# Kernel tuning notes

Hardware: AMD Instinct MI355X
Metric: run time of the kernel (lower is better)

## Reference

```python
import jax, jax.numpy as jnp
import numpy as np

NUM_ATTRS = 8    # A: number of attribute names in attr_map
NUM_VALS = 16    # V: number of distinct values per attribute


def setup_inputs() -> dict:
    key = jax.random.key(0)
    k1, k2 = jax.random.split(key)
    B, D = 2_000_000, 8
    predictions = jax.random.normal(k1, (B, D), dtype=jnp.float32)
    attr_vals = jax.random.randint(k2, (B, NUM_ATTRS), 0, NUM_VALS, dtype=jnp.int32)
    return {"predictions": predictions, "attr_vals": attr_vals}


def reference(predictions, attr_vals):
    B, A = attr_vals.shape
    V = NUM_VALS
    # per-node mean of sigmoid probs; stacking rows then .mean() == mean of per-node means
    per_node = jnp.mean(jax.nn.sigmoid(predictions), axis=1)  # [B]
    # flatten (attr, value) groups into A*V segments
    seg_ids = (attr_vals + jnp.arange(A, dtype=attr_vals.dtype)[None, :] * V).reshape(-1)  # [B*A]
    vals = jnp.broadcast_to(per_node[:, None], (B, A)).reshape(-1)  # [B*A]
    sums = jax.ops.segment_sum(vals, seg_ids, num_segments=A * V)
    counts = jax.ops.segment_sum(jnp.ones_like(vals), seg_ids, num_segments=A * V)
    means = (sums / jnp.maximum(counts, 1.0)).reshape(A, V)      # [A, V]
    present = (counts > 0).reshape(A, V)                          # [A, V]
    # pairwise squared diffs of group means within each attribute (i < j)
    diff = means[:, :, None] - means[:, None, :]                  # [A, V, V]
    triu = jnp.triu(jnp.ones((V, V), dtype=bool), k=1)
    pair_mask = present[:, :, None] & present[:, None, :] & triu[None, :, :]
    total_loss = jnp.sum(jnp.where(pair_mask, diff * diff, 0.0))
    num_comparisons = jnp.sum(pair_mask)
    return jnp.where(num_comparisons > 0, total_loss / num_comparisons, 0.0)
```

## Files before the change

### kernel.cpp

```cpp
#include <hip/hip_runtime.h>

#define NA 8
#define NV 16
#define NS (NA * NV)
#define NW 4
#define FIX_SHIFT 43
#define FIX_MASK ((1ULL << FIX_SHIFT) - 1)
#define FIX_SCALE 2147483648.0f


__device__ __forceinline__ float sig(float x) {
    return __builtin_amdgcn_rcpf(1.0f + __expf(-x));
}

__device__ __forceinline__ void process_chunk(
    float4 p, int4 a, int lane, unsigned long long* __restrict__ hw)
{
    float hs = sig(p.x) + sig(p.y) + sig(p.z) + sig(p.w);
    float s  = hs + __shfl_xor(hs, 1, 64);
    float per_node = s * 0.125f;
    unsigned int fixed = (unsigned int)(per_node * FIX_SCALE);
    unsigned long long add = (1ULL << FIX_SHIFT) | (unsigned long long)fixed;
    const int abase = (lane & 1) << 2;
    atomicAdd(&hw[((abase + 0) << 4) + a.x], add);
    atomicAdd(&hw[((abase + 1) << 4) + a.y], add);
    atomicAdd(&hw[((abase + 2) << 4) + a.z], add);
    atomicAdd(&hw[((abase + 3) << 4) + a.w], add);
}

__global__ __launch_bounds__(256) void k1_accum(
    const float* __restrict__ preds,
    const int*   __restrict__ attrs,
    unsigned long long* __restrict__ partials,
    int B, int nb)
{
    __shared__ unsigned long long h[NW][NS];
    for (int i = threadIdx.x; i < NW * NS; i += 256)
        ((unsigned long long*)h)[i] = 0ULL;
    __syncthreads();

    const int lane = threadIdx.x & 63;
    const int wave = threadIdx.x >> 6;
    unsigned long long* __restrict__ hw = h[wave];

    const float4* __restrict__ p4 = (const float4*)preds;
    const int4*   __restrict__ a4 = (const int4*)attrs;

    const int gw      = blockIdx.x * NW + wave;
    const int nwv     = nb * NW;
    const int nchunks = B >> 5;

    int c = gw;
    if (c < nchunks) {
        float4 p = p4[(size_t)c * 64 + lane];
        int4   a = a4[(size_t)c * 64 + lane];
        for (;;) {
            const int  cn   = c + nwv;
            const bool more = (cn < nchunks);
            float4 pn; int4 an;
            if (more) {
                pn = p4[(size_t)cn * 64 + lane];
                an = a4[(size_t)cn * 64 + lane];
            }
            process_chunk(p, a, lane, hw);
            if (!more) break;
            p = pn; a = an; c = cn;
        }
    }

    const int rem = B & 31;
    if (rem && blockIdx.x == 0 && wave == 0 && lane < rem * 2) {
        const size_t base = (size_t)(B >> 5) * 64;
        float4 p = p4[base + lane];
        int4   a = a4[base + lane];
        process_chunk(p, a, lane, hw);
    }
    __syncthreads();

    if (threadIdx.x < NS) {
        unsigned long long m = h[0][threadIdx.x] + h[1][threadIdx.x]
                             + h[2][threadIdx.x] + h[3][threadIdx.x];
        partials[(size_t)threadIdx.x * nb + blockIdx.x] = m;
    }
}

__global__ __launch_bounds__(256) void k2_reduce(
    const unsigned long long* __restrict__ partials,
    double* __restrict__ means,
    int*    __restrict__ pres,
    int nb)
{
    const int s = blockIdx.x;
    unsigned long long sum = 0ULL;
    unsigned int cnt = 0u;
    for (int b = threadIdx.x; b < nb; b += 256) {
        unsigned long long p = partials[(size_t)s * nb + b];
        cnt += (unsigned int)(p >> FIX_SHIFT);
        sum += (p & FIX_MASK);
    }
    for (int off = 32; off > 0; off >>= 1) {
        sum += __shfl_down(sum, off, 64);
        cnt += __shfl_down(cnt, off, 64);
    }
    __shared__ unsigned long long ws_[4];
    __shared__ unsigned int wc_[4];
    const int wave = threadIdx.x >> 6;
    if ((threadIdx.x & 63) == 0) { ws_[wave] = sum; wc_[wave] = cnt; }
    __syncthreads();
    if (threadIdx.x == 0) {
        unsigned long long S = ws_[0] + ws_[1] + ws_[2] + ws_[3];
        unsigned int C = wc_[0] + wc_[1] + wc_[2] + wc_[3];
        means[s] = C ? ((double)S * (1.0 / (double)FIX_SCALE)) / (double)C : 0.0;
        pres[s]  = C ? 1 : 0;
    }
}

__global__ __launch_bounds__(128) void k3_finalize(
    const double* __restrict__ means,
    const int*    __restrict__ pres,
    float* __restrict__ out)
{
    __shared__ double s_mean[NS];
    __shared__ int    s_pres[NS];
    const int t = threadIdx.x;
    s_mean[t] = means[t];
    s_pres[t] = pres[t];
    __syncthreads();

    const int a = t >> 4;
    const int i = t & (NV - 1);
    double loss = 0.0;
    int    ncmp = 0;
    if (s_pres[t]) {
        const double mi = s_mean[t];
        for (int j = i + 1; j < NV; ++j) {
            const int sj = a * NV + j;
            if (s_pres[sj]) {
                const double d = mi - s_mean[sj];
                loss += d * d;
                ncmp += 1;
            }
        }
    }
    for (int off = 32; off > 0; off >>= 1) {
        loss += __shfl_down(loss, off, 64);
        ncmp += __shfl_down(ncmp, off, 64);
    }
    __shared__ double w_loss[2];
    __shared__ int    w_ncmp[2];
    const int wave = t >> 6;
    if ((t & 63) == 0) { w_loss[wave] = loss; w_ncmp[wave] = ncmp; }
    __syncthreads();
    if (t == 0) {
        const double total = w_loss[0] + w_loss[1];
        const int    n     = w_ncmp[0] + w_ncmp[1];
        out[0] = (n > 0) ? (float)(total / (double)n) : 0.0f;
    }
}

extern "C" void kernel_launch(void* const* d_in, const int* in_sizes, int n_in,
                              void* d_out, int out_size, void* d_ws, size_t ws_size,
                              hipStream_t stream) {
    const float* preds = (const float*)d_in[0];
    const int*   attrs = (const int*)d_in[1];
    float*       out   = (float*)d_out;

    const int B = in_sizes[1] / NA;

    const size_t tail = NS * sizeof(double) + NS * sizeof(int);
    int nb = 2048;
    while (nb > 512 &&
           ws_size < (size_t)NS * nb * sizeof(unsigned long long) + tail) {
        nb >>= 1;
    }

    unsigned long long* partials = (unsigned long long*)d_ws;
    double* means = (double*)((char*)d_ws + (size_t)NS * nb * sizeof(unsigned long long));
    int*    pres  = (int*)(means + NS);

    k1_accum<<<nb, 256, 0, stream>>>(preds, attrs, partials, B, nb);
    k2_reduce<<<NS, 256, 0, stream>>>(partials, means, pres, nb);
    k3_finalize<<<1, 128, 0, stream>>>(means, pres, out);
}
```

Measured before the change: 153.9 us.

## Use per-lane private LDS histograms instead of shared 64-bit atomics

Measured after the change: 199.6 us. 29.7% more time.

```diff
diff --git a/kernel.cpp b/kernel.cpp
--- a/kernel.cpp
+++ b/kernel.cpp
@@ -3,10 +3,12 @@
 #define NA 8
 #define NV 16
 #define NS (NA * NV)
-#define NW 4
+#define NW 2
 #define FIX_SHIFT 43
 #define FIX_MASK ((1ULL << FIX_SHIFT) - 1)
-#define FIX_SCALE 2147483648.0f
+#define FIX_SCALE 2097152.0f
+#define CNT_SH 26
+#define CELL_MASK ((1u << CNT_SH) - 1)
 
 
 __device__ __forceinline__ float sig(float x) {
@@ -14,34 +16,41 @@
 }
 
 __device__ __forceinline__ void process_chunk(
-    float4 p, int4 a, int lane, unsigned long long* __restrict__ hw)
+    float4 p, int4 a, unsigned int* __restrict__ Hw)
 {
     float hs = sig(p.x) + sig(p.y) + sig(p.z) + sig(p.w);
     float s  = hs + __shfl_xor(hs, 1, 64);
-    float per_node = s * 0.125f;
-    unsigned int fixed = (unsigned int)(per_node * FIX_SCALE);
-    unsigned long long add = (1ULL << FIX_SHIFT) | (unsigned long long)fixed;
-    const int abase = (lane & 1) << 2;
-    atomicAdd(&hw[((abase + 0) << 4) + a.x], add);
-    atomicAdd(&hw[((abase + 1) << 4) + a.y], add);
-    atomicAdd(&hw[((abase + 2) << 4) + a.z], add);
-    atomicAdd(&hw[((abase + 3) << 4) + a.w], add);
-}
-
-__global__ __launch_bounds__(256) void k1_accum(
+    unsigned int fixed = (unsigned int)(s * 262144.0f);
+    unsigned int add   = (1u << CNT_SH) | fixed;
+    int i0 =        ((unsigned)a.x << 6);
+    int i1 = 1024 + ((unsigned)a.y << 6);
+    int i2 = 2048 + ((unsigned)a.z << 6);
+    int i3 = 3072 + ((unsigned)a.w << 6);
+    unsigned int c0 = Hw[i0], c1 = Hw[i1], c2 = Hw[i2], c3 = Hw[i3];
+    Hw[i0] = c0 + add;
+    Hw[i1] = c1 + add;
+    Hw[i2] = c2 + add;
+    Hw[i3] = c3 + add;
+}
+
+__global__ __launch_bounds__(128) void k1_accum(
     const float* __restrict__ preds,
     const int*   __restrict__ attrs,
     unsigned long long* __restrict__ partials,
     int B, int nb)
 {
-    __shared__ unsigned long long h[NW][NS];
-    for (int i = threadIdx.x; i < NW * NS; i += 256)
-        ((unsigned long long*)h)[i] = 0ULL;
-    __syncthreads();
+    __shared__ unsigned int H[NW * 64 * 64];
+    __shared__ unsigned long long P[NW * NS];
 
     const int lane = threadIdx.x & 63;
     const int wave = threadIdx.x >> 6;
-    unsigned long long* __restrict__ hw = h[wave];
+    unsigned int* __restrict__ Hw = H + wave * 4096 + lane;
+
+    {
+        uint4* Hi = (uint4*)(H + wave * 4096);
+        uint4 z; z.x = z.y = z.z = z.w = 0u;
+        for (int i = lane; i < 1024; i += 64) Hi[i] = z;
+    }
 
     const float4* __restrict__ p4 = (const float4*)preds;
     const int4*   __restrict__ a4 = (const int4*)attrs;
@@ -52,19 +61,41 @@
 
     int c = gw;
     if (c < nchunks) {
-        float4 p = p4[(size_t)c * 64 + lane];
-        int4   a = a4[(size_t)c * 64 + lane];
+        float4 P0, P1, P2, P3;
+        int4   A0, A1, A2, A3;
+        {
+            int c1 = (c + 1 * nwv < nchunks) ? c + 1 * nwv : c;
+            int c2 = (c + 2 * nwv < nchunks) ? c + 2 * nwv : c;
+            int c3 = (c + 3 * nwv < nchunks) ? c + 3 * nwv : c;
+            P0 = p4[(size_t)c  * 64 + lane];  A0 = a4[(size_t)c  * 64 + lane];
+            P1 = p4[(size_t)c1 * 64 + lane];  A1 = a4[(size_t)c1 * 64 + lane];
+            P2 = p4[(size_t)c2 * 64 + lane];  A2 = a4[(size_t)c2 * 64 + lane];
+            P3 = p4[(size_t)c3 * 64 + lane];  A3 = a4[(size_t)c3 * 64 + lane];
+        }
         for (;;) {
-            const int  cn   = c + nwv;
-            const bool more = (cn < nchunks);
-            float4 pn; int4 an;
-            if (more) {
-                pn = p4[(size_t)cn * 64 + lane];
-                an = a4[(size_t)cn * 64 + lane];
-            }
-            process_chunk(p, a, lane, hw);
-            if (!more) break;
-            p = pn; a = an; c = cn;
+            process_chunk(P0, A0, Hw);
+            { int cn = c + 4 * nwv;
+              if (cn < nchunks) { P0 = p4[(size_t)cn * 64 + lane];
+                                  A0 = a4[(size_t)cn * 64 + lane]; } }
+            c += nwv; if (c >= nchunks) break;
+
+            process_chunk(P1, A1, Hw);
+            { int cn = c + 4 * nwv;
+              if (cn < nchunks) { P1 = p4[(size_t)cn * 64 + lane];
+                                  A1 = a4[(size_t)cn * 64 + lane]; } }
+            c += nwv; if (c >= nchunks) break;
+
+            process_chunk(P2, A2, Hw);
+            { int cn = c + 4 * nwv;
+              if (cn < nchunks) { P2 = p4[(size_t)cn * 64 + lane];
+                                  A2 = a4[(size_t)cn * 64 + lane]; } }
+            c += nwv; if (c >= nchunks) break;
+
+            process_chunk(P3, A3, Hw);
+            { int cn = c + 4 * nwv;
+              if (cn < nchunks) { P3 = p4[(size_t)cn * 64 + lane];
+                                  A3 = a4[(size_t)cn * 64 + lane]; } }
+            c += nwv; if (c >= nchunks) break;
         }
     }
 
@@ -73,13 +104,27 @@
         const size_t base = (size_t)(B >> 5) * 64;
         float4 p = p4[base + lane];
         int4   a = a4[base + lane];
-        process_chunk(p, a, lane, hw);
+        process_chunk(p, a, Hw);
+    }
+
+    for (int s = 0; s < 64; ++s) {
+        unsigned int cell = Hw[s * 64];
+        unsigned int cnt = cell >> CNT_SH;
+        unsigned int fix = cell & CELL_MASK;
+        #pragma unroll
+        for (int m = 2; m <= 32; m <<= 1) {
+            cnt += __shfl_xor(cnt, m, 64);
+            fix += __shfl_xor(fix, m, 64);
+        }
+        if (lane < 2) {
+            P[wave * NS + s + (lane << 6)] =
+                ((unsigned long long)cnt << FIX_SHIFT) | (unsigned long long)fix;
+        }
     }
     __syncthreads();
 
     if (threadIdx.x < NS) {
-        unsigned long long m = h[0][threadIdx.x] + h[1][threadIdx.x]
-                             + h[2][threadIdx.x] + h[3][threadIdx.x];
+        unsigned long long m = P[threadIdx.x] + P[NS + threadIdx.x];
         partials[(size_t)threadIdx.x * nb + blockIdx.x] = m;
     }
 }
@@ -169,16 +214,13 @@
 
     const size_t tail = NS * sizeof(double) + NS * sizeof(int);
     int nb = 2048;
-    while (nb > 512 &&
-           ws_size < (size_t)NS * nb * sizeof(unsigned long long) + tail) {
-        nb >>= 1;
-    }
+    if (ws_size < (size_t)NS * nb * sizeof(unsigned long long) + tail) nb = 1024;
 
     unsigned long long* partials = (unsigned long long*)d_ws;
     double* means = (double*)((char*)d_ws + (size_t)NS * nb * sizeof(unsigned long long));
     int*    pres  = (int*)(means + NS);
 
-    k1_accum<<<nb, 256, 0, stream>>>(preds, attrs, partials, B, nb);
+    k1_accum<<<nb, 128, 0, stream>>>(preds, attrs, partials, B, nb);
     k2_reduce<<<NS, 256, 0, stream>>>(partials, means, pres, nb);
     k3_finalize<<<1, 128, 0, stream>>>(means, pres, out);
 }
```
